# Performance work log

Hardware: AMD Instinct MI355X
Metric: run time of the kernel (lower is better)

The kernel has to match this reference:

```python
import jax, jax.numpy as jnp
import numpy as np

B, T, N, C = 16, 12, 2048, 64
WIN = 3                    # window_size
F = 3                      # len(filters) branches
NW = T - WIN + 1           # number of windows = 10


def setup_inputs() -> dict:
    key = jax.random.key(0)
    k0, k1, k2, k3, k4 = jax.random.split(key, 5)
    data = jax.random.normal(k0, (B, T, N, C), jnp.float32)
    # scale adj so aggregated features stay O(1)
    adj = jax.random.normal(k1, (WIN * N, WIN * N), jnp.float32) / np.float32(np.sqrt(WIN * N))
    temporal_emb = jax.random.normal(k2, (1, T, 1, C), jnp.float32) * 0.1
    spatial_emb = jax.random.normal(k3, (1, 1, N, C), jnp.float32) * 0.1
    # per-window, per-filter GLU linear: C -> 2C
    W = jax.random.normal(k4, (NW, F, C, 2 * C), jnp.float32) / np.float32(np.sqrt(C))
    b = jnp.zeros((NW, F, 2 * C), jnp.float32)
    return {"data": data, "adj": adj, "temporal_emb": temporal_emb,
            "spatial_emb": spatial_emb, "W": W, "b": b}


def reference(data, adj, temporal_emb, spatial_emb, W, b):
    # data: (B,T,N,C); adj: (3N,3N)
    x = data + temporal_emb + spatial_emb                     # (B,T,N,C)
    # sliding windows of 3 time steps, flattened to 3N nodes  # (B,NW,3N,C)
    wins = jnp.stack([x[:, i:i + WIN].reshape(B, WIN * N, C) for i in range(NW)], axis=1)
    # only the middle N rows of the bmm output survive the mid-step slice,
    # so aggregate with just those rows of adj (same math, less work)
    adj_mid = adj[(WIN - 1) // 2 * N:(WIN + 1) // 2 * N]      # (N, 3N)
    agg = jnp.einsum('mn,bwnc->bwmc', adj_mid, wins)          # (B,NW,N,C)
    # per-window per-filter linear C -> 2C, then GLU
    pre = jnp.einsum('bwnc,wfcd->bwfnd', agg, W) + b[None, :, :, None, :]  # (B,NW,F,N,2C)
    lhs, rhs = jnp.split(pre, 2, axis=-1)
    glu = lhs * jax.nn.sigmoid(rhs)                           # (B,NW,F,N,C)
    # max over filter branches -> (B, T-2, N, C)
    return jnp.max(glu, axis=2)
```

## Files before the change

### kernel.cpp

```cpp
#include <hip/hip_runtime.h>
#include <hip/hip_bf16.h>

#define B_ 16
#define T_ 12
#define N_ 2048
#define C_ 64
#define NW_ 10
#define K_ 6144

#define NT2_ 96
#define ABUF_E 16384
#define BUF2_E 36864

typedef __attribute__((ext_vector_type(8))) short bf16x8;
typedef __attribute__((ext_vector_type(4))) float f32x4;

__device__ __forceinline__ unsigned short f2bf(float f) {
  union { float f; unsigned int u; } v; v.f = f;
  unsigned int u = v.u;
  return (unsigned short)((u + 0x7FFFu + ((u >> 16) & 1u)) >> 16);
}

__device__ __forceinline__ void gload16(const void* g, void* l) {
  __builtin_amdgcn_global_load_lds(
      (const __attribute__((address_space(1))) unsigned int*)g,
      (__attribute__((address_space(3))) unsigned int*)l, 16, 0, 0);
}

template<int N>
__device__ __forceinline__ void vmw() {
  if constexpr (N == 10)     asm volatile("s_waitcnt vmcnt(10)" ::: "memory");
  else if constexpr (N == 8) asm volatile("s_waitcnt vmcnt(8)" ::: "memory");
  else if constexpr (N == 5) asm volatile("s_waitcnt vmcnt(5)" ::: "memory");
  else if constexpr (N == 4) asm volatile("s_waitcnt vmcnt(4)" ::: "memory");
  else                       asm volatile("s_waitcnt vmcnt(0)" ::: "memory");
}

__global__ __launch_bounds__(256) void prep_x2(const float* __restrict__ data,
                                               const float* __restrict__ temb,
                                               const float* __restrict__ semb,
                                               unsigned short* __restrict__ xbt2) {
  int idx = blockIdx.x * 256 + threadIdx.x;
  int q = idx & 511;
  int btnb = idx >> 9;
  int nb = btnb & 31;
  int bt = btnb >> 5;
  int t = bt % T_;
  int o = q >> 6, c = q & 63;
  int n0 = nb * 64 + o * 8;
  float te = temb[t * C_ + c];
  union { unsigned short s[8]; uint4 v; } pk;
#pragma unroll
  for (int e = 0; e < 8; ++e) {
    int n = n0 + e;
    float d = data[((size_t)bt * N_ + n) * C_ + c];
    float se = semb[(size_t)n * C_ + c];
    pk.s[e] = f2bf(d + te + se);
  }
  *(uint4*)(xbt2 + (size_t)idx * 8) = pk.v;
}

__global__ __launch_bounds__(256) void prep_adj2(const float* __restrict__ adj,
                                                 unsigned short* __restrict__ adjb2) {
  int idx = blockIdx.x * 256 + threadIdx.x;
  int s = idx & 2047;
  int bmt = idx >> 11;
  int t = bmt % NT2_;
  int bm = bmt / NT2_;
  int r = s & 15;
  int o = (s >> 4) & 7;
  int rg = s >> 7;
  int m = bm * 256 + rg * 16 + r;
  int k = t * 64 + o * 8;
  const float* src = adj + ((size_t)(N_ + m)) * K_ + k;
  float4 a = *(const float4*)src;
  float4 b4 = *(const float4*)(src + 4);
  union { unsigned short s8[8]; uint4 v; } pk;
  pk.s8[0] = f2bf(a.x);  pk.s8[1] = f2bf(a.y);  pk.s8[2] = f2bf(a.z);  pk.s8[3] = f2bf(a.w);
  pk.s8[4] = f2bf(b4.x); pk.s8[5] = f2bf(b4.y); pk.s8[6] = f2bf(b4.z); pk.s8[7] = f2bf(b4.w);
  *(uint4*)(adjb2 + (size_t)idx * 8) = pk.v;
}

__global__ __launch_bounds__(256) void prep_w(const float* __restrict__ W,
                                              unsigned short* __restrict__ wbt) {
  int idx = blockIdx.x * 256 + threadIdx.x;
  int c = idx & 63;
  int d = (idx >> 6) & 127;
  int wf = idx >> 13;
  float v = W[((size_t)wf * 64 + c) * 128 + d];
  wbt[idx] = f2bf(v);
}

struct SegCtx {
  const unsigned short* Abase;
  const unsigned short* Xroot;
  int lane, wid, wm, wn, l4, l15, fbase, bOffLane;
};

__device__ __forceinline__ void stage_group(const SegCtx& s, unsigned short* lds, int t, int kh) {
  unsigned short* buf = lds + (t & 1) * BUF2_E;
  int tp = t >> 5, nn = t & 31;
#pragma unroll
  for (int ci = 0; ci < 2; ++ci) {
    int rg = s.wid * 2 + ci;
    int off = (rg * 128 + kh * 64) * 8;
    gload16(s.Abase + (size_t)t * ABUF_E + off + s.lane * 8, buf + off);
  }
  unsigned short* Bb = buf + ABUF_E;
  const unsigned short* Xr = s.Xroot + ((size_t)tp * 32 + nn) * 4096;
  int c0 = (s.wid < 4) ? s.wid * 3 : 12 + (s.wid - 4) * 2;
  int nc = (s.wid < 4) ? 3 : 2;
  for (int ci = 0; ci < nc; ++ci) {
    int cg = c0 + ci;
    gload16(Xr + (size_t)(cg >> 2) * 131072 + kh * 2048 + (cg & 3) * 128 + s.bOffLane,
            Bb + cg * 1024 + kh * 512);
  }
}

__device__ __forceinline__ void vm_steady(const SegCtx& s) {
  if (s.wid < 4) vmw<10>(); else vmw<8>();
}
__device__ __forceinline__ void vm_tail(const SegCtx& s) {
  if (s.wid < 4) vmw<5>(); else vmw<4>();
}

template<int KK>
__device__ __forceinline__ void phase_body(const SegCtx& s, unsigned short* lds, int t,
                                           f32x4 (&acc)[8][5]) {
  if constexpr (KK == 0) { if (t + 1 < NT2_) stage_group(s, lds, t + 1, 1); }
  else                   { if (t + 2 < NT2_) stage_group(s, lds, t + 2, 0); }
  const unsigned short* buf = lds + (t & 1) * BUF2_E;
  const unsigned short* Ab = buf;
  const unsigned short* Bb = buf + ABUF_E;
  bf16x8 bfv[5], af[8];
#pragma unroll
  for (int c = 0; c < 5; ++c)
    bfv[c] = *(const bf16x8*)(Bb + (s.wn * 5 + c) * 1024 + KK * 512 + s.fbase);
#pragma unroll
  for (int i = 0; i < 8; ++i)
    af[i] = *(const bf16x8*)(Ab + (s.wm * 8 + i) * 1024 + KK * 512 + s.fbase);
  __builtin_amdgcn_s_setprio(1);
#pragma unroll
  for (int i = 0; i < 8; ++i)
#pragma unroll
    for (int c = 0; c < 5; ++c)
      acc[i][c] = __builtin_amdgcn_mfma_f32_16x16x32_bf16(af[i], bfv[c], acc[i][c], 0, 0, 0);
  __builtin_amdgcn_s_setprio(0);
  if constexpr (KK == 0) {
    if (t == NT2_ - 1) vmw<0>(); else vm_steady(s);
    __builtin_amdgcn_s_barrier();
    __builtin_amdgcn_sched_barrier(0);
  } else {
    if (t < NT2_ - 2) vm_steady(s);
    else if (t == NT2_ - 2) vm_tail(s);
    if (t < NT2_ - 1) {
      __builtin_amdgcn_s_barrier();
      __builtin_amdgcn_sched_barrier(0);
    }
  }
}

__global__ __launch_bounds__(512, 2) void gemm_agg(const unsigned short* __restrict__ adjb2,
                                                   const unsigned short* __restrict__ xbt2,
                                                   unsigned short* __restrict__ aggb) {
  __shared__ __align__(16) unsigned short lds[2 * BUF2_E];
  int bid = blockIdx.x;
  int bm = bid & 7;
  int rest = bid >> 3;
  int seg = rest & 1;
  int b = rest >> 1;
  int w0 = seg * 5;
  int tid = threadIdx.x;
  SegCtx s;
  s.lane = tid & 63; s.wid = tid >> 6;
  s.wm = s.wid >> 2; s.wn = s.wid & 3;
  s.l4 = s.lane >> 4; s.l15 = s.lane & 15;
  s.fbase = s.l4 * 128 + s.l15 * 8;
  s.bOffLane = s.l4 * 512 + s.l15 * 8;
  s.Abase = adjb2 + (size_t)bm * NT2_ * ABUF_E;
  s.Xroot = xbt2 + ((size_t)(b * T_ + w0)) * C_ * N_;

  f32x4 acc[8][5];
#pragma unroll
  for (int i = 0; i < 8; ++i)
#pragma unroll
    for (int c = 0; c < 5; ++c) acc[i][c] = (f32x4)0.f;

  __builtin_amdgcn_sched_barrier(0);
  stage_group(s, lds, 0, 0);
  stage_group(s, lds, 0, 1);
  stage_group(s, lds, 1, 0);
  vm_steady(s);
  __builtin_amdgcn_s_barrier();
  __builtin_amdgcn_sched_barrier(0);

  for (int t = 0; t < NT2_; ++t) {
    phase_body<0>(s, lds, t, acc);
    phase_body<1>(s, lds, t, acc);
  }

  unsigned short* Ob0 = aggb + (size_t)(b * NW_ + w0) * N_ * C_;
#pragma unroll
  for (int c = 0; c < 5; ++c) {
    int col = s.wn * 80 + c * 16 + s.l15;
    int g = col >> 6, cc = col & 63;
    unsigned short* Ob = Ob0 + (size_t)g * N_ * C_ + cc;
#pragma unroll
    for (int i = 0; i < 8; ++i) {
      int n0 = bm * 256 + s.wm * 128 + i * 16 + s.l4 * 4;
#pragma unroll
      for (int q = 0; q < 4; ++q)
        Ob[(size_t)(n0 + q) * C_] = f2bf(acc[i][c][q]);
    }
  }
}

__global__ __launch_bounds__(256) void glu_out(const unsigned short* __restrict__ aggb,
                                               const unsigned short* __restrict__ wbt,
                                               const float* __restrict__ bias,
                                               float* __restrict__ out) {
  __shared__ __align__(16) unsigned short sW[3 * 128 * 64];
  int bn = blockIdx.x, bw = blockIdx.y;
  int w = bw % NW_;
  int tid = threadIdx.x, lane = tid & 63, wid = tid >> 6;
  int lrow8 = lane >> 3, jl = lane & 7;
  int l15 = lane & 15, l4 = lane >> 4;
  const unsigned short* Wsrc = wbt + (size_t)w * 3 * 128 * 64;
  for (int ci = 0; ci < 12; ++ci) {
    int chunk = wid * 12 + ci;
    int row = chunk * 8 + lrow8;
    int jg = jl ^ (row & 7);
    gload16(Wsrc + (size_t)row * 64 + jg * 8, &sW[chunk * 512]);
  }
  const unsigned short* Abase = aggb + ((size_t)bw * N_ + bn * 128 + wid * 32) * C_;
  bf16x8 af[2][2];
  for (int i = 0; i < 2; ++i)
    for (int kh = 0; kh < 2; ++kh)
      af[i][kh] = *(const bf16x8*)(Abase + (size_t)(i * 16 + l15) * C_ + kh * 32 + l4 * 8);
  __syncthreads();

  float omax[2][4][4];
  for (int i = 0; i < 2; ++i)
    for (int j = 0; j < 4; ++j)
      for (int r = 0; r < 4; ++r) omax[i][j][r] = -INFINITY;

  for (int f = 0; f < 3; ++f) {
    f32x4 acc[2][8];
    for (int i = 0; i < 2; ++i)
      for (int j = 0; j < 8; ++j) acc[i][j] = (f32x4)0.f;
    for (int kh = 0; kh < 2; ++kh) {
      int gchunk = kh * 4 + l4;
      for (int j = 0; j < 8; ++j) {
        int row = f * 128 + j * 16 + l15;
        int ch = gchunk ^ (row & 7);
        bf16x8 bfr = *(const bf16x8*)&sW[row * 64 + ch * 8];
        for (int i = 0; i < 2; ++i)
          acc[i][j] = __builtin_amdgcn_mfma_f32_16x16x32_bf16(af[i][kh], bfr, acc[i][j], 0, 0, 0);
      }
    }
    for (int j = 0; j < 4; ++j) {
      float bl = bias[(w * 3 + f) * 128 + j * 16 + l15];
      float br = bias[(w * 3 + f) * 128 + 64 + j * 16 + l15];
      for (int i = 0; i < 2; ++i)
        for (int r = 0; r < 4; ++r) {
          float lhs = acc[i][j][r] + bl;
          float rhs = acc[i][j + 4][r] + br;
          float g = lhs / (1.f + __expf(-rhs));
          omax[i][j][r] = fmaxf(omax[i][j][r], g);
        }
    }
  }
  float* Obase = out + ((size_t)bw * N_ + bn * 128 + wid * 32) * C_;
  for (int i = 0; i < 2; ++i)
    for (int j = 0; j < 4; ++j)
      for (int r = 0; r < 4; ++r)
        Obase[(size_t)(i * 16 + l4 * 4 + r) * C_ + j * 16 + l15] = omax[i][j][r];
}

extern "C" void kernel_launch(void* const* d_in, const int* in_sizes, int n_in,
                              void* d_out, int out_size, void* d_ws, size_t ws_size,
                              hipStream_t stream) {
  const float* data = (const float*)d_in[0];
  const float* adj  = (const float*)d_in[1];
  const float* temb = (const float*)d_in[2];
  const float* semb = (const float*)d_in[3];
  const float* W    = (const float*)d_in[4];
  const float* bias = (const float*)d_in[5];
  float* out = (float*)d_out;

  char* ws = (char*)d_ws;
  unsigned short* xbt2  = (unsigned short*)ws;
  unsigned short* adjb2 = (unsigned short*)(ws + 50331648);
  unsigned short* wbt   = (unsigned short*)(ws + 75497472);
  unsigned short* aggb  = (unsigned short*)(ws + 75988992);

  hipLaunchKernelGGL(prep_x2,   dim3(12288), dim3(256), 0, stream, data, temb, semb, xbt2);
  hipLaunchKernelGGL(prep_adj2, dim3(6144),  dim3(256), 0, stream, adj, adjb2);
  hipLaunchKernelGGL(prep_w,    dim3(960),   dim3(256), 0, stream, W, wbt);
  hipLaunchKernelGGL(gemm_agg,  dim3(256),   dim3(512), 0, stream, adjb2, xbt2, aggb);
  hipLaunchKernelGGL(glu_out,   dim3(16, 160), dim3(256), 0, stream, aggb, wbt, bias, out);
}
```

Measured before the change: 323.5 us.

## Shrink gemm_agg tiles to 128 rows with 4 waves and triple-buffered B

```diff
diff --git a/kernel.cpp b/kernel.cpp
--- a/kernel.cpp
+++ b/kernel.cpp
@@ -10,7 +10,9 @@
 
 #define NT2_ 96
 #define ABUF_E 16384
-#define BUF2_E 36864
+#define NT32 192
+#define ABUF32 4096
+#define BBUF32 10240
 
 typedef __attribute__((ext_vector_type(8))) short bf16x8;
 typedef __attribute__((ext_vector_type(4))) float f32x4;
@@ -29,11 +31,8 @@
 
 template<int N>
 __device__ __forceinline__ void vmw() {
-  if constexpr (N == 10)     asm volatile("s_waitcnt vmcnt(10)" ::: "memory");
-  else if constexpr (N == 8) asm volatile("s_waitcnt vmcnt(8)" ::: "memory");
-  else if constexpr (N == 5) asm volatile("s_waitcnt vmcnt(5)" ::: "memory");
-  else if constexpr (N == 4) asm volatile("s_waitcnt vmcnt(4)" ::: "memory");
-  else                       asm volatile("s_waitcnt vmcnt(0)" ::: "memory");
+  if constexpr (N == 5) asm volatile("s_waitcnt vmcnt(5)" ::: "memory");
+  else                  asm volatile("s_waitcnt vmcnt(0)" ::: "memory");
 }
 
 __global__ __launch_bounds__(256) void prep_x2(const float* __restrict__ data,
@@ -94,51 +93,47 @@
 struct SegCtx {
   const unsigned short* Abase;
   const unsigned short* Xroot;
-  int lane, wid, wm, wn, l4, l15, fbase, bOffLane;
+  int lane, wid, l4, l15, fbase, bOffLane, wid5;
 };
 
-__device__ __forceinline__ void stage_group(const SegCtx& s, unsigned short* lds, int t, int kh) {
-  unsigned short* buf = lds + (t & 1) * BUF2_E;
-  int tp = t >> 5, nn = t & 31;
+__device__ __forceinline__ void stage_A(const SegCtx& s, unsigned short* ldsA, int u) {
+  unsigned short* dst = ldsA + (u & 1) * ABUF32;
+  const unsigned short* src = s.Abase + (size_t)(u >> 1) * ABUF_E + (u & 1) * 512;
 #pragma unroll
   for (int ci = 0; ci < 2; ++ci) {
     int rg = s.wid * 2 + ci;
-    int off = (rg * 128 + kh * 64) * 8;
-    gload16(s.Abase + (size_t)t * ABUF_E + off + s.lane * 8, buf + off);
-  }
-  unsigned short* Bb = buf + ABUF_E;
-  const unsigned short* Xr = s.Xroot + ((size_t)tp * 32 + nn) * 4096;
-  int c0 = (s.wid < 4) ? s.wid * 3 : 12 + (s.wid - 4) * 2;
-  int nc = (s.wid < 4) ? 3 : 2;
-  for (int ci = 0; ci < nc; ++ci) {
-    int cg = c0 + ci;
-    gload16(Xr + (size_t)(cg >> 2) * 131072 + kh * 2048 + (cg & 3) * 128 + s.bOffLane,
-            Bb + cg * 1024 + kh * 512);
-  }
-}
-
-__device__ __forceinline__ void vm_steady(const SegCtx& s) {
-  if (s.wid < 4) vmw<10>(); else vmw<8>();
-}
-__device__ __forceinline__ void vm_tail(const SegCtx& s) {
-  if (s.wid < 4) vmw<5>(); else vmw<4>();
-}
-
-template<int KK>
-__device__ __forceinline__ void phase_body(const SegCtx& s, unsigned short* lds, int t,
-                                           f32x4 (&acc)[8][5]) {
-  if constexpr (KK == 0) { if (t + 1 < NT2_) stage_group(s, lds, t + 1, 1); }
-  else                   { if (t + 2 < NT2_) stage_group(s, lds, t + 2, 0); }
-  const unsigned short* buf = lds + (t & 1) * BUF2_E;
-  const unsigned short* Ab = buf;
-  const unsigned short* Bb = buf + ABUF_E;
-  bf16x8 bfv[5], af[8];
+    gload16(src + rg * 1024 + s.lane * 8, dst + rg * 512);
+  }
+}
+
+__device__ __forceinline__ void stage_B(const SegCtx& s, unsigned short* ldsB, int u, int dbuf) {
+  unsigned short* dst = ldsB + dbuf * BBUF32;
+  int t96 = u >> 1, kh = u & 1;
+  const unsigned short* Xr = s.Xroot + (size_t)t96 * 4096 + kh * 2048;
+#pragma unroll
+  for (int ci = 0; ci < 5; ++ci) {
+    int cg = s.wid5 + ci;
+    gload16(Xr + (size_t)(cg >> 2) * 131072 + (cg & 3) * 128 + s.bOffLane,
+            dst + cg * 512);
+  }
+}
+
+template<int BR>
+__device__ __forceinline__ void phase32(const SegCtx& s, unsigned short* ldsA,
+                                        unsigned short* ldsB, int u, f32x4 (&acc)[8][5]) {
+  constexpr int SB = (BR + 2) % 3;
+  if (u + 1 < NT32) stage_A(s, ldsA, u + 1);
+  if (u + 2 < NT32) stage_B(s, ldsB, u + 2, SB);
+  __builtin_amdgcn_sched_barrier(0);
+  const unsigned short* Ab = ldsA + (u & 1) * ABUF32;
+  const unsigned short* Bb = ldsB + BR * BBUF32;
+  bf16x8 af[8], bfv[5];
 #pragma unroll
   for (int c = 0; c < 5; ++c)
-    bfv[c] = *(const bf16x8*)(Bb + (s.wn * 5 + c) * 1024 + KK * 512 + s.fbase);
+    bfv[c] = *(const bf16x8*)(Bb + (s.wid5 + c) * 512 + s.fbase);
 #pragma unroll
   for (int i = 0; i < 8; ++i)
-    af[i] = *(const bf16x8*)(Ab + (s.wm * 8 + i) * 1024 + KK * 512 + s.fbase);
+    af[i] = *(const bf16x8*)(Ab + i * 512 + s.fbase);
   __builtin_amdgcn_s_setprio(1);
 #pragma unroll
   for (int i = 0; i < 8; ++i)
@@ -146,38 +141,32 @@
     for (int c = 0; c < 5; ++c)
       acc[i][c] = __builtin_amdgcn_mfma_f32_16x16x32_bf16(af[i], bfv[c], acc[i][c], 0, 0, 0);
   __builtin_amdgcn_s_setprio(0);
-  if constexpr (KK == 0) {
-    if (t == NT2_ - 1) vmw<0>(); else vm_steady(s);
+  if (u < NT32 - 2) vmw<5>();
+  else if (u == NT32 - 2) vmw<0>();
+  if (u < NT32 - 1) {
     __builtin_amdgcn_s_barrier();
     __builtin_amdgcn_sched_barrier(0);
-  } else {
-    if (t < NT2_ - 2) vm_steady(s);
-    else if (t == NT2_ - 2) vm_tail(s);
-    if (t < NT2_ - 1) {
-      __builtin_amdgcn_s_barrier();
-      __builtin_amdgcn_sched_barrier(0);
-    }
-  }
-}
-
-__global__ __launch_bounds__(512, 2) void gemm_agg(const unsigned short* __restrict__ adjb2,
+  }
+}
+
+__global__ __launch_bounds__(256, 2) void gemm_agg(const unsigned short* __restrict__ adjb2,
                                                    const unsigned short* __restrict__ xbt2,
                                                    unsigned short* __restrict__ aggb) {
-  __shared__ __align__(16) unsigned short lds[2 * BUF2_E];
+  __shared__ __align__(16) unsigned short ldsA[2 * ABUF32];
+  __shared__ __align__(16) unsigned short ldsB[3 * BBUF32];
   int bid = blockIdx.x;
-  int bm = bid & 7;
-  int rest = bid >> 3;
-  int seg = rest & 1;
-  int b = rest >> 1;
-  int w0 = seg * 5;
+  int bm = bid & 15;
+  int bs = bid >> 4;
+  int b = bs >> 1;
+  int w0 = (bs & 1) * 5;
   int tid = threadIdx.x;
   SegCtx s;
   s.lane = tid & 63; s.wid = tid >> 6;
-  s.wm = s.wid >> 2; s.wn = s.wid & 3;
   s.l4 = s.lane >> 4; s.l15 = s.lane & 15;
   s.fbase = s.l4 * 128 + s.l15 * 8;
   s.bOffLane = s.l4 * 512 + s.l15 * 8;
-  s.Abase = adjb2 + (size_t)bm * NT2_ * ABUF_E;
+  s.wid5 = s.wid * 5;
+  s.Abase = adjb2 + (size_t)(bm >> 1) * NT2_ * ABUF_E + (bm & 1) * 8192;
   s.Xroot = xbt2 + ((size_t)(b * T_ + w0)) * C_ * N_;
 
   f32x4 acc[8][5];
@@ -187,27 +176,28 @@
     for (int c = 0; c < 5; ++c) acc[i][c] = (f32x4)0.f;
 
   __builtin_amdgcn_sched_barrier(0);
-  stage_group(s, lds, 0, 0);
-  stage_group(s, lds, 0, 1);
-  stage_group(s, lds, 1, 0);
-  vm_steady(s);
+  stage_A(s, ldsA, 0);
+  stage_B(s, ldsB, 0, 0);
+  stage_B(s, ldsB, 1, 1);
+  vmw<5>();
   __builtin_amdgcn_s_barrier();
   __builtin_amdgcn_sched_barrier(0);
 
-  for (int t = 0; t < NT2_; ++t) {
-    phase_body<0>(s, lds, t, acc);
-    phase_body<1>(s, lds, t, acc);
+  for (int u = 0; u < NT32; u += 3) {
+    phase32<0>(s, ldsA, ldsB, u, acc);
+    phase32<1>(s, ldsA, ldsB, u + 1, acc);
+    phase32<2>(s, ldsA, ldsB, u + 2, acc);
   }
 
   unsigned short* Ob0 = aggb + (size_t)(b * NW_ + w0) * N_ * C_;
 #pragma unroll
   for (int c = 0; c < 5; ++c) {
-    int col = s.wn * 80 + c * 16 + s.l15;
+    int col = s.wid * 80 + c * 16 + s.l15;
     int g = col >> 6, cc = col & 63;
     unsigned short* Ob = Ob0 + (size_t)g * N_ * C_ + cc;
 #pragma unroll
     for (int i = 0; i < 8; ++i) {
-      int n0 = bm * 256 + s.wm * 128 + i * 16 + s.l4 * 4;
+      int n0 = bm * 128 + i * 16 + s.l4 * 4;
 #pragma unroll
       for (int q = 0; q < 4; ++q)
         Ob[(size_t)(n0 + q) * C_] = f2bf(acc[i][c][q]);
@@ -297,6 +287,6 @@
   hipLaunchKernelGGL(prep_x2,   dim3(12288), dim3(256), 0, stream, data, temb, semb, xbt2);
   hipLaunchKernelGGL(prep_adj2, dim3(6144),  dim3(256), 0, stream, adj, adjb2);
   hipLaunchKernelGGL(prep_w,    dim3(960),   dim3(256), 0, stream, W, wbt);
-  hipLaunchKernelGGL(gemm_agg,  dim3(256),   dim3(512), 0, stream, adjb2, xbt2, aggb);
+  hipLaunchKernelGGL(gemm_agg,  dim3(512),   dim3(256), 0, stream, adjb2, xbt2, aggb);
   hipLaunchKernelGGL(glu_out,   dim3(16, 160), dim3(256), 0, stream, aggb, wbt, bias, out);
 }
```

After: 936.8 us. +189.6%, slower.
